# Kernel tuning notes

Hardware: AMD Instinct MI355X
Metric: run time of the kernel (lower is better)

Reference implementation:

```python
import jax, jax.numpy as jnp
import numpy as np

E = 1024
H = 16
D = E // H  # head dim


def setup_inputs() -> dict:
    key = jax.random.key(0)
    ks = jax.random.split(key, 8)
    N, L = 4, 2048
    x = jax.random.normal(ks[0], (N, L, E), dtype=jnp.float32)
    attn_mask = jnp.zeros((N, L), dtype=jnp.float32)  # additive mask
    s = 0.02
    Wq = jax.random.normal(ks[1], (E, E), dtype=jnp.float32) * s
    bq = jnp.zeros((E,), dtype=jnp.float32)
    Wk = jax.random.normal(ks[2], (E, E), dtype=jnp.float32) * s
    bk = jnp.zeros((E,), dtype=jnp.float32)
    Wv = jax.random.normal(ks[3], (E, E), dtype=jnp.float32) * s
    bv = jnp.zeros((E,), dtype=jnp.float32)
    return {"x": x, "attn_mask": attn_mask, "Wq": Wq, "bq": bq,
            "Wk": Wk, "bk": bk, "Wv": Wv, "bv": bv}


def _to_heads(t):
    N, L, _ = t.shape
    return t.reshape(N, L, H, D).transpose(0, 2, 1, 3)  # [N,H,L,D]


def reference(x, attn_mask, Wq, bq, Wk, bk, Wv, bv):
    # Linear projections (torch Linear: x @ W.T + b)
    Q = _to_heads(x @ Wq.T + bq) * (1.0 / jnp.sqrt(jnp.float32(D)))
    K = _to_heads(x @ Wk.T + bk)
    V = _to_heads(x @ Wv.T + bv)
    scores = jnp.einsum('nhqd,nhkd->nhqk', Q, K) + attn_mask[:, None, None, :]
    attn = jax.nn.softmax(scores, axis=-1)  # dropout p=0 -> identity
    out = jnp.einsum('nhqk,nhkd->nhqd', attn, V)  # [N,H,L,D]
    N, _, L, _ = out.shape
    return out.transpose(0, 2, 1, 3).reshape(N, L, E)
```

## Files before the change

kernel.cpp:

```cpp
#include <hip/hip_runtime.h>

#define DEV __device__ __forceinline__

typedef unsigned short u16;
typedef __attribute__((ext_vector_type(8))) __bf16 bf16x8;
typedef __attribute__((ext_vector_type(4))) float f32x4;
typedef __attribute__((ext_vector_type(16))) float f32x16;

#define LOG2E 1.44269504088896340736f

DEV u16 f2bf(float f) {
  union { float f; unsigned u; } v; v.f = f;
  unsigned r = v.u + 0x7FFFu + ((v.u >> 16) & 1u);
  return (u16)(r >> 16);
}

DEV float exp2_fast(float x) {
#if __has_builtin(__builtin_amdgcn_exp2f)
  return __builtin_amdgcn_exp2f(x);
#else
  float r;
  asm volatile("v_exp_f32 %0, %1" : "=v"(r) : "v"(x));
  return r;
#endif
}

DEV float xor32_f(float v) { return __shfl_xor(v, 32, 64); }
DEV unsigned xor32_u(unsigned v) {
  return (unsigned)__shfl_xor((int)v, 32, 64);
}
DEV unsigned cvtpk(float lo, float hi) {
  unsigned r;
  asm volatile("v_cvt_pk_bf16_f32 %0, %1, %2" : "=v"(r) : "v"(lo), "v"(hi));
  return r;
}
DEV float bperm_f(int srclane, float v) {
  union { float f; int i; } u;
  u.f = v;
  u.i = __builtin_amdgcn_ds_bpermute(srclane * 4, u.i);
  return u.f;
}

template <typename T>
DEV void gload_lds16(const T* g, T* l) {
  __builtin_amdgcn_global_load_lds(
      (const __attribute__((address_space(1))) void*)(g),
      (__attribute__((address_space(3))) void*)(l),
      16, 0, 0);
}

DEV bf16x8 ldfrag(const u16* p) { return *(const bf16x8*)p; }

__global__ __launch_bounds__(256) void cast_kernel(const float* __restrict__ in,
                                                   u16* __restrict__ out, int n8) {
  int i = blockIdx.x * blockDim.x + threadIdx.x;
  if (i >= n8) return;
  float4 a = ((const float4*)in)[2 * i];
  float4 b = ((const float4*)in)[2 * i + 1];
  uint4 o;
  o.x = (unsigned)f2bf(a.x) | ((unsigned)f2bf(a.y) << 16);
  o.y = (unsigned)f2bf(a.z) | ((unsigned)f2bf(a.w) << 16);
  o.z = (unsigned)f2bf(b.x) | ((unsigned)f2bf(b.y) << 16);
  o.w = (unsigned)f2bf(b.z) | ((unsigned)f2bf(b.w) << 16);
  ((uint4*)out)[i] = o;
}

__global__ __launch_bounds__(256) void mask_scale(const float* __restrict__ in,
                                                  float* __restrict__ outp, int n) {
  int i = blockIdx.x * blockDim.x + threadIdx.x;
  if (i < n) outp[i] = in[i] * LOG2E;
}

__global__ __launch_bounds__(256) void qkv_gemm(
    const u16* __restrict__ xb, const u16* __restrict__ wb,
    const float* __restrict__ bq, const float* __restrict__ bk, const float* __restrict__ bv,
    u16* __restrict__ qb, u16* __restrict__ kb, u16* __restrict__ vb) {
  __shared__ u16 As[128 * 64];
  __shared__ u16 Bs[128 * 64];
  const int t = threadIdx.x, lane = t & 63, w = t >> 6;
  const int wm = w >> 1, wn = w & 1;
  const int m0 = blockIdx.x * 128;
  const int cb = blockIdx.y;
  const int wsel = cb >> 3;
  const int n0 = (cb & 7) * 128;
  const u16* W = wb + wsel * (1024 * 1024);
  const float* bias = (wsel == 0) ? bq : (wsel == 1) ? bk : bv;
  u16* dst = (wsel == 0) ? qb : (wsel == 1) ? kb : vb;
  const float scale = (wsel == 0) ? 0.125f * LOG2E : 1.0f;

  f32x4 acc[4][4];
  const f32x4 z4 = {0.f, 0.f, 0.f, 0.f};
  for (int i = 0; i < 4; ++i)
    for (int j = 0; j < 4; ++j) acc[i][j] = z4;

  const int srow = w * 32 + (lane >> 3);
  const int scol = (lane & 7) * 8;

  for (int k0 = 0; k0 < 1024; k0 += 64) {
    __syncthreads();
    for (int i = 0; i < 4; ++i) {
      gload_lds16(xb + (m0 + srow + i * 8) * 1024 + k0 + scol, &As[w * 2048 + i * 512]);
      gload_lds16(W + (n0 + srow + i * 8) * 1024 + k0 + scol, &Bs[w * 2048 + i * 512]);
    }
    __syncthreads();
    for (int ks = 0; ks < 2; ++ks) {
      bf16x8 a[4], b[4];
      for (int mi = 0; mi < 4; ++mi)
        a[mi] = ldfrag(&As[(wm * 64 + mi * 16 + (lane & 15)) * 64 + ks * 32 + (lane >> 4) * 8]);
      for (int ni = 0; ni < 4; ++ni)
        b[ni] = ldfrag(&Bs[(wn * 64 + ni * 16 + (lane & 15)) * 64 + ks * 32 + (lane >> 4) * 8]);
      for (int mi = 0; mi < 4; ++mi)
        for (int ni = 0; ni < 4; ++ni)
          acc[mi][ni] = __builtin_amdgcn_mfma_f32_16x16x32_bf16(a[mi], b[ni], acc[mi][ni], 0, 0, 0);
    }
  }
  for (int ni = 0; ni < 4; ++ni) {
    int col = n0 + wn * 64 + ni * 16 + (lane & 15);
    float bv_ = bias[col];
    int h = col >> 6, d = col & 63;
    for (int mi = 0; mi < 4; ++mi) {
      for (int r = 0; r < 4; ++r) {
        int gm = m0 + wm * 64 + mi * 16 + (lane >> 4) * 4 + r;
        int nn = gm >> 11, lq = gm & 2047;
        float val = acc[mi][ni][r] * scale + bv_;
        dst[(((nn << 4) + h) * 2048 + lq) * 64 + d] = f2bf(val);
      }
    }
  }
}

__global__ __launch_bounds__(256) void transpose_v(const u16* __restrict__ vb,
                                                   u16* __restrict__ vtb) {
  __shared__ u16 T[64][68];
  const int t = threadIdx.x;
  const int l0 = blockIdx.x * 64;
  const int head = blockIdx.y;
  const u16* src = vb + head * (2048 * 64) + l0 * 64;
  for (int c = t; c < 512; c += 256) {
    int l = c >> 3, dd = (c & 7) * 8;
    uint4 v = *(const uint4*)(src + l * 64 + dd);
    u16* d = &T[l][dd];
    ((uint2*)d)[0] = make_uint2(v.x, v.y);
    ((uint2*)d)[1] = make_uint2(v.z, v.w);
  }
  __syncthreads();
  u16* dsth = vtb + head * (64 * 2048);
  for (int c = t; c < 512; c += 256) {
    int d = c >> 3, lp = (c & 7) * 8;
    u16 tmp[8];
    for (int j = 0; j < 8; ++j) tmp[j] = T[lp + j][d];
    uint4 o;
    o.x = (unsigned)tmp[0] | ((unsigned)tmp[1] << 16);
    o.y = (unsigned)tmp[2] | ((unsigned)tmp[3] << 16);
    o.z = (unsigned)tmp[4] | ((unsigned)tmp[5] << 16);
    o.w = (unsigned)tmp[6] | ((unsigned)tmp[7] << 16);
    *(uint4*)(dsth + d * 2048 + l0 + lp) = o;
  }
}

__global__ __launch_bounds__(256) void flash_attn(
    const u16* __restrict__ qb, const u16* __restrict__ kb, const u16* __restrict__ vtb,
    const float* __restrict__ mlog, float* __restrict__ out) {
  __shared__ u16 SM[4][64 * 64];

  const int t = threadIdx.x, lane = t & 63, w = t >> 6;
  const int hi = lane >> 5, l31 = lane & 31;
  const int q0 = blockIdx.x * 128;
  const int head = blockIdx.y;
  const int n = head >> 4, h = head & 15;

  const u16* qh = qb + head * (2048 * 64);
  const u16* kh = kb + head * (2048 * 64);
  const u16* vth = vtb + head * (64 * 2048);
  const float* mrow = mlog + n * 2048;

  const int srow8 = lane >> 3;
  const int scolsw = ((lane & 7) ^ srow8) * 8;
  const int rsw = (lane & 7) * 8;
  int fcolB[4];
  for (int dk = 0; dk < 4; ++dk) fcolB[dk] = (16 * dk + 8 * hi) ^ rsw;

  u16* QL = &SM[0][0];
  for (int i = 0; i < 4; ++i)
    gload_lds16(qh + (q0 + w * 32 + i * 8 + srow8) * 64 + scolsw, &QL[(w * 32 + i * 8) * 64]);
  __syncthreads();
  bf16x8 qf[4];
  for (int dk = 0; dk < 4; ++dk)
    qf[dk] = ldfrag(&QL[(w * 32 + l31) * 64 + fcolB[dk]]);
  __syncthreads();

  {
    gload_lds16(kh + (w * 16 + srow8) * 64 + scolsw, &SM[0][w * 1024]);
    gload_lds16(kh + (w * 16 + 8 + srow8) * 64 + scolsw, &SM[0][w * 1024 + 512]);
    for (int i = 0; i < 2; ++i) {
      int dbase = w * 16 + i * 8;
      gload_lds16(vth + (dbase + srow8) * 2048 + scolsw, &SM[2][dbase * 64]);
    }
  }

  f32x16 o0, o1;
  for (int r = 0; r < 16; ++r) { o0[r] = 0.f; o1[r] = 0.f; }
  float m_ = -1e30f, lp = 0.f;

  for (int tt = 0; tt < 32; ++tt) {
    const int cur = tt & 1;
    const int kv0 = tt * 64;
    __syncthreads();

    if (tt < 31) {
      const int kv1 = kv0 + 64;
      const u16* ksrc = kh + kv1 * 64;
      gload_lds16(ksrc + (w * 16 + srow8) * 64 + scolsw, &SM[cur ^ 1][w * 1024]);
      gload_lds16(ksrc + (w * 16 + 8 + srow8) * 64 + scolsw, &SM[cur ^ 1][w * 1024 + 512]);
      for (int i = 0; i < 2; ++i) {
        int dbase = w * 16 + i * 8;
        gload_lds16(vth + (dbase + srow8) * 2048 + kv1 + scolsw, &SM[2 + (cur ^ 1)][dbase * 64]);
      }
    }
    const u16* Kc = &SM[cur][0];
    const u16* Vc = &SM[2 + cur][0];

    f32x16 s1, s2;
    {
      const float* mb = mrow + kv0 + 4 * hi;
      for (int mq = 0; mq < 4; ++mq) {
        f32x4 ma = *(const f32x4*)(mb + 8 * mq);
        f32x4 mc = *(const f32x4*)(mb + 32 + 8 * mq);
        for (int e = 0; e < 4; ++e) { s1[4 * mq + e] = ma[e]; s2[4 * mq + e] = mc[e]; }
      }
    }
    for (int dk = 0; dk < 4; ++dk) {
      bf16x8 k0 = ldfrag(&Kc[l31 * 64 + fcolB[dk]]);
      bf16x8 k1 = ldfrag(&Kc[(32 + l31) * 64 + fcolB[dk]]);
      s1 = __builtin_amdgcn_mfma_f32_32x32x16_bf16(k0, qf[dk], s1, 0, 0, 0);
      s2 = __builtin_amdgcn_mfma_f32_32x32x16_bf16(k1, qf[dk], s2, 0, 0, 0);
    }

    float pml = s1[0];
    for (int r = 1; r < 16; ++r) pml = fmaxf(pml, s1[r]);
    for (int r = 0; r < 16; ++r) pml = fmaxf(pml, s2[r]);

    if (!__all(pml <= m_ + 8.f)) {
      float pm = fmaxf(pml, xor32_f(pml));
      float nm = fmaxf(m_, pm);
      float sc = exp2_fast(m_ - nm);
      m_ = nm;
      lp *= sc;
      for (int r = 0; r < 16; ++r) {
        float scr = bperm_f((r & 3) + 8 * (r >> 2) + 4 * hi, sc);
        o0[r] *= scr;
        o1[r] *= scr;
      }
    }

    for (int r = 0; r < 16; ++r) {
      s1[r] = exp2_fast(s1[r] - m_);
      s2[r] = exp2_fast(s2[r] - m_);
      lp += s1[r] + s2[r];
    }

    unsigned raw[16];
    for (int mq = 0; mq < 8; ++mq) {
      raw[mq] = cvtpk(s1[2 * mq], s1[2 * mq + 1]);
      raw[8 + mq] = cvtpk(s2[2 * mq], s2[2 * mq + 1]);
    }
    union { unsigned u[16]; bf16x8 v[4]; } pw;
    for (int g = 0; g < 4; ++g) {
      unsigned a0 = raw[4 * g], a1 = raw[4 * g + 1];
      unsigned a2 = raw[4 * g + 2], a3 = raw[4 * g + 3];
      unsigned p0 = xor32_u(a0), p1 = xor32_u(a1);
      unsigned p2 = xor32_u(a2), p3 = xor32_u(a3);
      pw.u[4 * g + 0] = hi ? p2 : a0;
      pw.u[4 * g + 1] = hi ? p3 : a1;
      pw.u[4 * g + 2] = hi ? a2 : p0;
      pw.u[4 * g + 3] = hi ? a3 : p1;
    }

    for (int kc = 0; kc < 4; ++kc) {
      bf16x8 bv0 = ldfrag(&Vc[l31 * 64 + fcolB[kc]]);
      bf16x8 bv1 = ldfrag(&Vc[(32 + l31) * 64 + fcolB[kc]]);
      o0 = __builtin_amdgcn_mfma_f32_32x32x16_bf16(pw.v[kc], bv0, o0, 0, 0, 0);
      o1 = __builtin_amdgcn_mfma_f32_32x32x16_bf16(pw.v[kc], bv1, o1, 0, 0, 0);
    }
  }

  float lpf = lp + xor32_f(lp);
  float inv = 1.0f / lpf;
  for (int r = 0; r < 16; ++r) {
    int qrow = (r & 3) + 8 * (r >> 2) + 4 * hi;
    float invr = bperm_f(qrow, inv);
    int q = q0 + w * 32 + qrow;
    float* ob = out + (n * 2048 + q) * 1024 + h * 64;
    ob[l31] = o0[r] * invr;
    ob[32 + l31] = o1[r] * invr;
  }
}

extern "C" void kernel_launch(void* const* d_in, const int* in_sizes, int n_in,
                              void* d_out, int out_size, void* d_ws, size_t ws_size,
                              hipStream_t stream) {
  const float* x = (const float*)d_in[0];
  const float* mask = (const float*)d_in[1];
  const float* Wq = (const float*)d_in[2];
  const float* bq = (const float*)d_in[3];
  const float* Wk = (const float*)d_in[4];
  const float* bk = (const float*)d_in[5];
  const float* Wv = (const float*)d_in[6];
  const float* bv = (const float*)d_in[7];
  float* out = (float*)d_out;

  u16* xb = (u16*)d_ws;
  u16* wb = xb + 8192 * 1024;
  u16* qb = wb + 3 * 1024 * 1024;
  u16* kb = qb + 64 * 2048 * 64;
  u16* vb = kb + 64 * 2048 * 64;
  u16* vtb = vb + 64 * 2048 * 64;
  float* mlog = (float*)wb;

  cast_kernel<<<8192 * 1024 / 8 / 256, 256, 0, stream>>>(x, xb, 8192 * 1024 / 8);
  cast_kernel<<<1024 * 1024 / 8 / 256, 256, 0, stream>>>(Wq, wb, 1024 * 1024 / 8);
  cast_kernel<<<1024 * 1024 / 8 / 256, 256, 0, stream>>>(Wk, wb + 1024 * 1024, 1024 * 1024 / 8);
  cast_kernel<<<1024 * 1024 / 8 / 256, 256, 0, stream>>>(Wv, wb + 2 * 1024 * 1024, 1024 * 1024 / 8);
  qkv_gemm<<<dim3(64, 24), 256, 0, stream>>>(xb, wb, bq, bk, bv, qb, kb, vb);
  mask_scale<<<(4 * 2048 + 255) / 256, 256, 0, stream>>>(mask, mlog, 4 * 2048);
  transpose_v<<<dim3(32, 64), 256, 0, stream>>>(vb, vtb);
  flash_attn<<<dim3(16, 64), 256, 0, stream>>>(qb, kb, vtb, mlog, out);
}
```

Baseline: 217.8 us.

## Fuse prep kernels, write V transposed from GEMM, tune flash attention inner loop

Merges the four cast launches and the mask scaling into a single prep kernel, and has the QKV GEMM epilogue write V directly in transposed layout so the separate transpose kernel disappears. The flash attention grid is flattened and swizzled so neighbouring blocks share heads, MFMA sections are bracketed with s_setprio, and the row-max and row-sum reductions become tree reductions. The xor32 permutes in the P repack drop from four to two per group. The cost is a more scattered V epilogue store (ushort4 strided by 2048) and more register pressure from the unrolled reductions.

```diff
diff --git a/kernel.cpp b/kernel.cpp
--- a/kernel.cpp
+++ b/kernel.cpp
@@ -51,30 +51,48 @@
 
 DEV bf16x8 ldfrag(const u16* p) { return *(const bf16x8*)p; }
 
-__global__ __launch_bounds__(256) void cast_kernel(const float* __restrict__ in,
-                                                   u16* __restrict__ out, int n8) {
-  int i = blockIdx.x * blockDim.x + threadIdx.x;
-  if (i >= n8) return;
-  float4 a = ((const float4*)in)[2 * i];
-  float4 b = ((const float4*)in)[2 * i + 1];
+DEV void cast8(const float* __restrict__ in, u16* __restrict__ out) {
+  float4 a = ((const float4*)in)[0];
+  float4 b = ((const float4*)in)[1];
   uint4 o;
   o.x = (unsigned)f2bf(a.x) | ((unsigned)f2bf(a.y) << 16);
   o.y = (unsigned)f2bf(a.z) | ((unsigned)f2bf(a.w) << 16);
   o.z = (unsigned)f2bf(b.x) | ((unsigned)f2bf(b.y) << 16);
   o.w = (unsigned)f2bf(b.z) | ((unsigned)f2bf(b.w) << 16);
-  ((uint4*)out)[i] = o;
-}
-
-__global__ __launch_bounds__(256) void mask_scale(const float* __restrict__ in,
-                                                  float* __restrict__ outp, int n) {
-  int i = blockIdx.x * blockDim.x + threadIdx.x;
-  if (i < n) outp[i] = in[i] * LOG2E;
+  *(uint4*)out = o;
+}
+
+__global__ __launch_bounds__(256) void prep_kernel(
+    const float* __restrict__ x, const float* __restrict__ Wq,
+    const float* __restrict__ Wk, const float* __restrict__ Wv,
+    const float* __restrict__ mask,
+    u16* __restrict__ xb, u16* __restrict__ wb, float* __restrict__ mlog) {
+  const int i = blockIdx.x * 256 + threadIdx.x;
+  const int NX = 8192 * 1024 / 8;
+  const int NW = 1024 * 1024 / 8;
+  if (i < NX) {
+    cast8(x + (long)i * 8, xb + (long)i * 8);
+  } else if (i < NX + 3 * NW) {
+    int j = i - NX;
+    int sel = j / NW;
+    int jj = j - sel * NW;
+    const float* W = (sel == 0) ? Wq : (sel == 1) ? Wk : Wv;
+    cast8(W + (long)jj * 8, wb + (long)j * 8);
+  } else {
+    int j = i - NX - 3 * NW;
+    float4 a = ((const float4*)mask)[2 * j];
+    float4 b = ((const float4*)mask)[2 * j + 1];
+    a.x *= LOG2E; a.y *= LOG2E; a.z *= LOG2E; a.w *= LOG2E;
+    b.x *= LOG2E; b.y *= LOG2E; b.z *= LOG2E; b.w *= LOG2E;
+    ((float4*)mlog)[2 * j] = a;
+    ((float4*)mlog)[2 * j + 1] = b;
+  }
 }
 
 __global__ __launch_bounds__(256) void qkv_gemm(
     const u16* __restrict__ xb, const u16* __restrict__ wb,
     const float* __restrict__ bq, const float* __restrict__ bk, const float* __restrict__ bv,
-    u16* __restrict__ qb, u16* __restrict__ kb, u16* __restrict__ vb) {
+    u16* __restrict__ qb, u16* __restrict__ kb, u16* __restrict__ vtb) {
   __shared__ u16 As[128 * 64];
   __shared__ u16 Bs[128 * 64];
   const int t = threadIdx.x, lane = t & 63, w = t >> 6;
@@ -85,7 +103,6 @@
   const int n0 = (cb & 7) * 128;
   const u16* W = wb + wsel * (1024 * 1024);
   const float* bias = (wsel == 0) ? bq : (wsel == 1) ? bk : bv;
-  u16* dst = (wsel == 0) ? qb : (wsel == 1) ? kb : vb;
   const float scale = (wsel == 0) ? 0.125f * LOG2E : 1.0f;
 
   f32x4 acc[4][4];
@@ -114,47 +131,37 @@
           acc[mi][ni] = __builtin_amdgcn_mfma_f32_16x16x32_bf16(a[mi], b[ni], acc[mi][ni], 0, 0, 0);
     }
   }
-  for (int ni = 0; ni < 4; ++ni) {
-    int col = n0 + wn * 64 + ni * 16 + (lane & 15);
-    float bv_ = bias[col];
-    int h = col >> 6, d = col & 63;
-    for (int mi = 0; mi < 4; ++mi) {
-      for (int r = 0; r < 4; ++r) {
-        int gm = m0 + wm * 64 + mi * 16 + (lane >> 4) * 4 + r;
+  if (wsel == 2) {
+    for (int ni = 0; ni < 4; ++ni) {
+      int col = n0 + wn * 64 + ni * 16 + (lane & 15);
+      float bv_ = bias[col];
+      int h = col >> 6, d = col & 63;
+      for (int mi = 0; mi < 4; ++mi) {
+        int gm = m0 + wm * 64 + mi * 16 + (lane >> 4) * 4;
         int nn = gm >> 11, lq = gm & 2047;
-        float val = acc[mi][ni][r] * scale + bv_;
-        dst[(((nn << 4) + h) * 2048 + lq) * 64 + d] = f2bf(val);
-      }
-    }
-  }
-}
-
-__global__ __launch_bounds__(256) void transpose_v(const u16* __restrict__ vb,
-                                                   u16* __restrict__ vtb) {
-  __shared__ u16 T[64][68];
-  const int t = threadIdx.x;
-  const int l0 = blockIdx.x * 64;
-  const int head = blockIdx.y;
-  const u16* src = vb + head * (2048 * 64) + l0 * 64;
-  for (int c = t; c < 512; c += 256) {
-    int l = c >> 3, dd = (c & 7) * 8;
-    uint4 v = *(const uint4*)(src + l * 64 + dd);
-    u16* d = &T[l][dd];
-    ((uint2*)d)[0] = make_uint2(v.x, v.y);
-    ((uint2*)d)[1] = make_uint2(v.z, v.w);
-  }
-  __syncthreads();
-  u16* dsth = vtb + head * (64 * 2048);
-  for (int c = t; c < 512; c += 256) {
-    int d = c >> 3, lp = (c & 7) * 8;
-    u16 tmp[8];
-    for (int j = 0; j < 8; ++j) tmp[j] = T[lp + j][d];
-    uint4 o;
-    o.x = (unsigned)tmp[0] | ((unsigned)tmp[1] << 16);
-    o.y = (unsigned)tmp[2] | ((unsigned)tmp[3] << 16);
-    o.z = (unsigned)tmp[4] | ((unsigned)tmp[5] << 16);
-    o.w = (unsigned)tmp[6] | ((unsigned)tmp[7] << 16);
-    *(uint4*)(dsth + d * 2048 + l0 + lp) = o;
+        ushort4 pk;
+        pk.x = f2bf(acc[mi][ni][0] + bv_);
+        pk.y = f2bf(acc[mi][ni][1] + bv_);
+        pk.z = f2bf(acc[mi][ni][2] + bv_);
+        pk.w = f2bf(acc[mi][ni][3] + bv_);
+        *(ushort4*)(vtb + ((long)((nn << 4) + h) * 64 + d) * 2048 + lq) = pk;
+      }
+    }
+  } else {
+    u16* dst = (wsel == 0) ? qb : kb;
+    for (int ni = 0; ni < 4; ++ni) {
+      int col = n0 + wn * 64 + ni * 16 + (lane & 15);
+      float bv_ = bias[col];
+      int h = col >> 6, d = col & 63;
+      for (int mi = 0; mi < 4; ++mi) {
+        for (int r = 0; r < 4; ++r) {
+          int gm = m0 + wm * 64 + mi * 16 + (lane >> 4) * 4 + r;
+          int nn = gm >> 11, lq = gm & 2047;
+          float val = acc[mi][ni][r] * scale + bv_;
+          dst[(((nn << 4) + h) * 2048 + lq) * 64 + d] = f2bf(val);
+        }
+      }
+    }
   }
 }
 
@@ -165,8 +172,10 @@
 
   const int t = threadIdx.x, lane = t & 63, w = t >> 6;
   const int hi = lane >> 5, l31 = lane & 31;
-  const int q0 = blockIdx.x * 128;
-  const int head = blockIdx.y;
+  const int bid = blockIdx.x;
+  const int swz = (bid & 7) * 128 + (bid >> 3);
+  const int q0 = (swz & 15) * 128;
+  const int head = swz >> 4;
   const int n = head >> 4, h = head & 15;
 
   const u16* qh = qb + head * (2048 * 64);
@@ -229,16 +238,23 @@
         for (int e = 0; e < 4; ++e) { s1[4 * mq + e] = ma[e]; s2[4 * mq + e] = mc[e]; }
       }
     }
+    __builtin_amdgcn_s_setprio(1);
     for (int dk = 0; dk < 4; ++dk) {
       bf16x8 k0 = ldfrag(&Kc[l31 * 64 + fcolB[dk]]);
       bf16x8 k1 = ldfrag(&Kc[(32 + l31) * 64 + fcolB[dk]]);
       s1 = __builtin_amdgcn_mfma_f32_32x32x16_bf16(k0, qf[dk], s1, 0, 0, 0);
       s2 = __builtin_amdgcn_mfma_f32_32x32x16_bf16(k1, qf[dk], s2, 0, 0, 0);
     }
-
-    float pml = s1[0];
-    for (int r = 1; r < 16; ++r) pml = fmaxf(pml, s1[r]);
-    for (int r = 0; r < 16; ++r) pml = fmaxf(pml, s2[r]);
+    __builtin_amdgcn_s_setprio(0);
+
+    float tm[16];
+#pragma unroll
+    for (int r = 0; r < 16; ++r) tm[r] = fmaxf(s1[r], s2[r]);
+#pragma unroll
+    for (int st = 8; st >= 1; st >>= 1)
+#pragma unroll
+      for (int r = 0; r < st; ++r) tm[r] = fmaxf(tm[r], tm[r + st]);
+    float pml = tm[0];
 
     if (!__all(pml <= m_ + 8.f)) {
       float pm = fmaxf(pml, xor32_f(pml));
@@ -253,35 +269,49 @@
       }
     }
 
+#pragma unroll
     for (int r = 0; r < 16; ++r) {
       s1[r] = exp2_fast(s1[r] - m_);
       s2[r] = exp2_fast(s2[r] - m_);
-      lp += s1[r] + s2[r];
-    }
+    }
+    float ts[16];
+#pragma unroll
+    for (int r = 0; r < 16; ++r) ts[r] = s1[r] + s2[r];
+#pragma unroll
+    for (int st = 8; st >= 1; st >>= 1)
+#pragma unroll
+      for (int r = 0; r < st; ++r) ts[r] += ts[r + st];
+    lp += ts[0];
 
     unsigned raw[16];
+#pragma unroll
     for (int mq = 0; mq < 8; ++mq) {
       raw[mq] = cvtpk(s1[2 * mq], s1[2 * mq + 1]);
       raw[8 + mq] = cvtpk(s2[2 * mq], s2[2 * mq + 1]);
     }
     union { unsigned u[16]; bf16x8 v[4]; } pw;
+#pragma unroll
     for (int g = 0; g < 4; ++g) {
       unsigned a0 = raw[4 * g], a1 = raw[4 * g + 1];
       unsigned a2 = raw[4 * g + 2], a3 = raw[4 * g + 3];
-      unsigned p0 = xor32_u(a0), p1 = xor32_u(a1);
-      unsigned p2 = xor32_u(a2), p3 = xor32_u(a3);
-      pw.u[4 * g + 0] = hi ? p2 : a0;
-      pw.u[4 * g + 1] = hi ? p3 : a1;
-      pw.u[4 * g + 2] = hi ? a2 : p0;
-      pw.u[4 * g + 3] = hi ? a3 : p1;
-    }
-
+      unsigned v0 = hi ? a0 : a2;
+      unsigned v1 = hi ? a1 : a3;
+      unsigned x0 = xor32_u(v0);
+      unsigned x1 = xor32_u(v1);
+      pw.u[4 * g + 0] = hi ? x0 : a0;
+      pw.u[4 * g + 1] = hi ? x1 : a1;
+      pw.u[4 * g + 2] = hi ? a2 : x0;
+      pw.u[4 * g + 3] = hi ? a3 : x1;
+    }
+
+    __builtin_amdgcn_s_setprio(1);
     for (int kc = 0; kc < 4; ++kc) {
       bf16x8 bv0 = ldfrag(&Vc[l31 * 64 + fcolB[kc]]);
       bf16x8 bv1 = ldfrag(&Vc[(32 + l31) * 64 + fcolB[kc]]);
       o0 = __builtin_amdgcn_mfma_f32_32x32x16_bf16(pw.v[kc], bv0, o0, 0, 0, 0);
       o1 = __builtin_amdgcn_mfma_f32_32x32x16_bf16(pw.v[kc], bv1, o1, 0, 0, 0);
     }
+    __builtin_amdgcn_s_setprio(0);
   }
 
   float lpf = lp + xor32_f(lp);
@@ -313,16 +343,10 @@
   u16* wb = xb + 8192 * 1024;
   u16* qb = wb + 3 * 1024 * 1024;
   u16* kb = qb + 64 * 2048 * 64;
-  u16* vb = kb + 64 * 2048 * 64;
-  u16* vtb = vb + 64 * 2048 * 64;
-  float* mlog = (float*)wb;
-
-  cast_kernel<<<8192 * 1024 / 8 / 256, 256, 0, stream>>>(x, xb, 8192 * 1024 / 8);
-  cast_kernel<<<1024 * 1024 / 8 / 256, 256, 0, stream>>>(Wq, wb, 1024 * 1024 / 8);
-  cast_kernel<<<1024 * 1024 / 8 / 256, 256, 0, stream>>>(Wk, wb + 1024 * 1024, 1024 * 1024 / 8);
-  cast_kernel<<<1024 * 1024 / 8 / 256, 256, 0, stream>>>(Wv, wb + 2 * 1024 * 1024, 1024 * 1024 / 8);
-  qkv_gemm<<<dim3(64, 24), 256, 0, stream>>>(xb, wb, bq, bk, bv, qb, kb, vb);
-  mask_scale<<<(4 * 2048 + 255) / 256, 256, 0, stream>>>(mask, mlog, 4 * 2048);
-  transpose_v<<<dim3(32, 64), 256, 0, stream>>>(vb, vtb);
-  flash_attn<<<dim3(16, 64), 256, 0, stream>>>(qb, kb, vtb, mlog, out);
-}
+  u16* vtb = kb + 64 * 2048 * 64;
+  float* mlog = (float*)(vtb + 64 * 2048 * 64);
+
+  prep_kernel<<<1442816 / 256, 256, 0, stream>>>(x, Wq, Wk, Wv, mask, xb, wb, mlog);
+  qkv_gemm<<<dim3(64, 24), 256, 0, stream>>>(xb, wb, bq, bk, bv, qb, kb, vtb);
+  flash_attn<<<1024, 256, 0, stream>>>(qb, kb, vtb, mlog, out);
+}
```

New measurement: 209.5 us. 1.04x faster.
